# Optimization experiments

Measured on AMD Instinct MI355X. Metric: run time of the kernel, lower is better.

Reference implementation:

```python
import jax, jax.numpy as jnp
import numpy as np

NEG_SLOPE = 0.2


def gatv2(x, src, dst, eattr, Wl, bl, Wr, br, We, att, bias, concat):
    # GATv2Conv (PyG semantics): message j->i, softmax over incoming edges of target i.
    n = x.shape[0]
    H, C = att.shape
    xl = (x @ Wl + bl).reshape(n, H, C)   # source transform lin_l
    xr = (x @ Wr + br).reshape(n, H, C)   # target transform lin_r
    xe = (eattr @ We).reshape(-1, H, C)   # edge transform lin_edge (no bias)
    g = jax.nn.leaky_relu(xl[src] + xr[dst] + xe, NEG_SLOPE)  # [E,H,C]
    e = jnp.einsum('ehc,hc->eh', g, att)                      # [E,H]
    m = jax.ops.segment_max(e, dst, num_segments=n)
    a = jnp.exp(e - m[dst])
    s = jax.ops.segment_sum(a, dst, num_segments=n)
    alpha = a / (s[dst] + 1e-16)                              # [E,H]
    out = jax.ops.segment_sum(alpha[:, :, None] * xl[src], dst, num_segments=n)
    out = out.reshape(n, H * C) if concat else out.mean(axis=1)
    return out + bias, alpha


def add_self_loops(src, dst, eattr, n):
    # PyG default: add_self_loops=True, fill_value='mean' for edge_attr
    loop = jnp.arange(n, dtype=src.dtype)
    fill = jnp.broadcast_to(eattr.mean(axis=0, keepdims=True), (n, eattr.shape[1]))
    return (jnp.concatenate([src, loop]), jnp.concatenate([dst, loop]),
            jnp.concatenate([eattr, fill], axis=0))


def setup_inputs() -> dict:
    key = jax.random.key(0)
    ks = iter(jax.random.split(key, 64))
    B, N, D = 4, 2048, 256
    n = B * N
    E = 131072
    H, C1 = 4, 64  # conv1: heads=4, out=hidden//heads=64 (concat -> 256)
    C2 = 256       # conv2: heads=4, out=256, concat=False (mean)
    IN1 = 770

    def rn(shape, s=0.05):
        return jax.random.normal(next(ks), shape, dtype=jnp.float32) * s

    inp = {
        'h': rn((B, N, D), 1.0), 'c_temp': rn((B, N, D), 1.0),
        'c_stereo': rn((B, N, D), 1.0), 'e_proj': rn((B, N, 2), 1.0),
        'f_Lt': rn((B, N, D), 1.0),
        'edges': jax.random.randint(next(ks), (2, E), 0, n, dtype=jnp.int64),
        'edge_attr': rn((E, 1), 1.0),
        # conv1
        'Wl1': rn((IN1, H * C1)), 'bl1': jnp.zeros((H * C1,), jnp.float32),
        'Wr1': rn((IN1, H * C1)), 'br1': jnp.zeros((H * C1,), jnp.float32),
        'We1': rn((1, H * C1)), 'att1': rn((H, C1)),
        'bias1': jnp.zeros((H * C1,), jnp.float32),
        # conv2
        'Wl2': rn((D, H * C2)), 'bl2': jnp.zeros((H * C2,), jnp.float32),
        'Wr2': rn((D, H * C2)), 'br2': jnp.zeros((H * C2,), jnp.float32),
        'We2': rn((1, H * C2)), 'att2': rn((H, C2)),
        'bias2': jnp.zeros((C2,), jnp.float32),
        # GRUCell ([in, 3H] layout; gate order r,z,n as in torch)
        'Wih': rn((D, 3 * D)), 'bih': jnp.zeros((3 * D,), jnp.float32),
        'Whh': rn((D, 3 * D)), 'bhh': jnp.zeros((3 * D,), jnp.float32),
        # heads
        'rW1': rn((D, 256)), 'rb1': jnp.zeros((256,), jnp.float32),
        'rW2': rn((256, 2)), 'rb2': jnp.zeros((2,), jnp.float32),
        'wW1': rn((D, 256)), 'wb1': jnp.zeros((256,), jnp.float32),
        'wW2': rn((256, 2)), 'wb2': jnp.zeros((2,), jnp.float32),
        'pW1': rn((D, 128)), 'pb1': jnp.zeros((128,), jnp.float32),
        'pW2': rn((128, 1)), 'pb2': jnp.zeros((1,), jnp.float32),
        'dW1': rn((D, 128)), 'db1': jnp.zeros((128,), jnp.float32),
        'dW2': rn((128, 1)), 'db2': jnp.zeros((1,), jnp.float32),
    }
    return inp


def reference(h, c_temp, c_stereo, e_proj, f_Lt, edges, edge_attr,
              Wl1, bl1, Wr1, br1, We1, att1, bias1,
              Wl2, bl2, Wr2, br2, We2, att2, bias2,
              Wih, bih, Whh, bhh,
              rW1, rb1, rW2, rb2, wW1, wb1, wW2, wb2,
              pW1, pb1, pW2, pb2, dW1, db1, dW2, db2):
    B, N, D = f_Lt.shape
    n = B * N
    x = jnp.concatenate([c_temp, c_stereo, e_proj, f_Lt], axis=-1).reshape(n, -1)

    src, dst, ea = add_self_loops(edges[0], edges[1], edge_attr, n)
    x1, _ = gatv2(x, src, dst, ea, Wl1, bl1, Wr1, br1, We1, att1, bias1, concat=True)
    x1 = jax.nn.relu(x1)
    x2, alpha = gatv2(x1, src, dst, ea, Wl2, bl2, Wr2, br2, We2, att2, bias2, concat=False)

    # GRUCell
    hf = h.reshape(n, -1)
    gi = x2 @ Wih + bih
    gh = hf @ Whh + bhh
    ir, iz, inew = jnp.split(gi, 3, axis=-1)
    hr, hz, hnew = jnp.split(gh, 3, axis=-1)
    r_g = jax.nn.sigmoid(ir + hr)
    z_g = jax.nn.sigmoid(iz + hz)
    n_g = jnp.tanh(inew + r_g * hnew)
    h_new = ((1.0 - z_g) * n_g + z_g * hf).reshape(B, N, D)

    res = jax.nn.relu(h_new @ rW1 + rb1) @ rW2 + rb2
    w = jax.nn.sigmoid(jax.nn.relu(h_new @ wW1 + wb1) @ wW2 + wb2)
    a_p = jax.nn.softplus(jax.nn.relu(h_new @ pW1 + pb1) @ pW2 + pb2).mean(axis=1)
    a_d = jax.nn.softplus(jax.nn.relu(h_new @ dW1 + db1) @ dW2 + db2)
    return (h_new, res, w, a_p, a_d)
```

## Files before the change

### kernel.cpp

```cpp
#include <hip/hip_runtime.h>
#include <hip/hip_bf16.h>
#include <cstdint>
#include <cstddef>

#define N_NODES 8192
#define E_RAW   131072
#define E_TOT   (E_RAW + N_NODES)
#define HEADS   4

typedef __attribute__((ext_vector_type(8))) __bf16 bf16x8;
typedef __attribute__((ext_vector_type(4))) float f32x4;
typedef __attribute__((ext_vector_type(2))) float f32x2;

__device__ __forceinline__ void gload_lds16(const void* g, void* lds) {
  __builtin_amdgcn_global_load_lds(
      (const __attribute__((address_space(1))) unsigned int*)g,
      (__attribute__((address_space(3))) unsigned int*)lds, 16, 0, 0);
}

__device__ __forceinline__ float bfbits2f(unsigned short u) {
  return __uint_as_float((unsigned)u << 16);
}
__device__ __forceinline__ unsigned short f2bfbits(float f) {
  __hip_bfloat16 b = __float2bfloat16(f);
  return *(unsigned short*)&b;
}
__device__ __forceinline__ f32x2 unpk2(unsigned u) {
  return (f32x2){__uint_as_float(u << 16), __uint_as_float(u & 0xffff0000u)};
}
__device__ __forceinline__ unsigned char f32_to_fp8(float v) {
  int r = __builtin_amdgcn_cvt_pk_fp8_f32(v, v, 0, false);
  return (unsigned char)(r & 0xff);
}

__device__ __forceinline__ int eSrc(const int* __restrict__ src, int e) {
  return (e < E_RAW) ? src[e] : (e - E_RAW);
}
__device__ __forceinline__ int eDst(const int* __restrict__ dst, int e) {
  return (e < E_RAW) ? dst[e] : (e - E_RAW);
}


__global__ __launch_bounds__(256) void prep_kernel(
    const float* __restrict__ ct, const float* __restrict__ cs,
    const float* __restrict__ ep, const float* __restrict__ fl,
    const float* __restrict__ h, const float* __restrict__ ea,
    const float* bl1, const float* br1, const float* bl2, const float* br2,
    const float* rb1, const float* wb1, const float* pb1, const float* db1,
    __hip_bfloat16* __restrict__ x, __hip_bfloat16* __restrict__ Hb,
    float* __restrict__ MP, int* __restrict__ icnt_ipos,
    float* B1, float* B2, float* BH) {
  int blk = blockIdx.x;
  int tid = threadIdx.x;
  if (blk < 8192) {
    int i = blk;
    for (int j = tid; j < 832; j += 256) {
      float v;
      if (j < 256)      v = ct[(size_t)i * 256 + j];
      else if (j < 512) v = cs[(size_t)i * 256 + (j - 256)];
      else if (j < 514) v = ep[(size_t)i * 2 + (j - 512)];
      else if (j < 770) v = fl[(size_t)i * 256 + (j - 514)];
      else              v = 0.f;
      x[(size_t)i * 832 + j] = __float2bfloat16(v);
    }
  } else if (blk < 9216) {
    size_t base = ((size_t)(blk - 8192) * 256 + tid) * 8;
    float4 a = *(const float4*)(h + base);
    float4 b = *(const float4*)(h + base + 4);
    unsigned short o[8];
    o[0]=f2bfbits(a.x); o[1]=f2bfbits(a.y); o[2]=f2bfbits(a.z); o[3]=f2bfbits(a.w);
    o[4]=f2bfbits(b.x); o[5]=f2bfbits(b.y); o[6]=f2bfbits(b.z); o[7]=f2bfbits(b.w);
    *(uint4*)((unsigned short*)Hb + base) = *(uint4*)o;
  } else if (blk < 9472) {
    __shared__ float sm[256];
    int bb = blk - 9216;
    float acc = 0.f;
    for (int i = bb * 256 + tid; i < E_RAW; i += 256 * 256) acc += ea[i];
    sm[tid] = acc; __syncthreads();
    for (int s = 128; s; s >>= 1) { if (tid < s) sm[tid] += sm[tid + s]; __syncthreads(); }
    if (tid == 0) MP[bb] = sm[0];
  } else if (blk < 9536) {
    int i = (blk - 9472) * 256 + tid;
    if (i < 2 * N_NODES) icnt_ipos[i] = 0;
  } else {
    int i = (blk - 9536) * 256 + tid;
    if (i < 512) B1[i] = (i < 256) ? bl1[i] : br1[i - 256];
    else if (i < 2560) { int k = i - 512; B2[k] = (k < 1024) ? bl2[k] : br2[k - 1024]; }
    else if (i < 3328) {
      int k = i - 2560;
      BH[k] = (k < 256) ? rb1[k] : (k < 512) ? wb1[k - 256] : (k < 640) ? pb1[k - 512] : db1[k - 640];
    }
  }
}


__global__ void csr_count(const int* __restrict__ dst, int* __restrict__ cnt) {
  int e = blockIdx.x * blockDim.x + threadIdx.x;
  if (e < E_TOT) atomicAdd(&cnt[eDst(dst, e)], 1);
}

__global__ __launch_bounds__(1024) void csr_scan(const int* __restrict__ cnt,
                                                 int* __restrict__ off,
                                                 float* __restrict__ MP) {
  __shared__ int part[1024];
  __shared__ float sm[256];
  int t = threadIdx.x;
  if (t < 256) sm[t] = MP[t];
  __syncthreads();
  for (int s = 128; s; s >>= 1) { if (t < s) sm[t] += sm[t + s]; __syncthreads(); }
  if (t == 0) MP[256] = sm[0] * (1.f / (float)E_RAW);
  int base = t * 8;
  int loc[8];
  int s = 0;
#pragma unroll
  for (int i = 0; i < 8; ++i) { loc[i] = s; s += cnt[base + i]; }
  part[t] = s; __syncthreads();
  for (int d = 1; d < 1024; d <<= 1) {
    int v = (t >= d) ? part[t - d] : 0;
    __syncthreads();
    part[t] += v;
    __syncthreads();
  }
  int pre = (t == 0) ? 0 : part[t - 1];
#pragma unroll
  for (int i = 0; i < 8; ++i) off[base + i] = pre + loc[i];
  if (t == 1023) off[8192] = part[1023];
}

__global__ void csr_fill(const int* __restrict__ src, const int* __restrict__ dst,
                         const float* __restrict__ ea, const float* __restrict__ eamean,
                         const int* __restrict__ off, int* __restrict__ pos,
                         int* __restrict__ srcn, float* __restrict__ eav) {
  int e = blockIdx.x * blockDim.x + threadIdx.x;
  if (e >= E_TOT) return;
  int d = eDst(dst, e);
  int p = off[d] + atomicAdd(&pos[d], 1);
  srcn[p] = eSrc(src, e);
  eav[p] = (e < E_RAW) ? ea[e] : eamean[0];
}


__global__ __launch_bounds__(256) void wt_all(
    const float* w0, const float* w1, const float* w2, const float* w3,
    const float* w4, const float* w5, const float* w6, const float* w7,
    const float* w8, const float* w9,
    __hip_bfloat16* WT1, __hip_bfloat16* WT2, __hip_bfloat16* WTih,
    __hip_bfloat16* WThh, __hip_bfloat16* WTh) {
  const int cum[10] = {208, 416, 672, 928, 1120, 1312, 1376, 1440, 1472, 1504};
  const int Kt[10]  = {770, 770, 256, 256, 256, 256, 256, 256, 256, 256};
  const int Nt[10]  = {256, 256, 1024, 1024, 768, 768, 256, 256, 128, 128};
  const int KPt[10] = {832, 832, 256, 256, 256, 256, 256, 256, 256, 256};
  const int n0t[10] = {0, 256, 0, 1024, 0, 0, 0, 256, 512, 640};
  int job = 0;
  while (blockIdx.x >= (unsigned)cum[job]) ++job;
  int lb = blockIdx.x - (job ? cum[job - 1] : 0);
  int K = Kt[job], N = Nt[job], KP = KPt[job], n0 = n0t[job];
  int tilesX = KP >> 5;
  int k0 = (lb % tilesX) * 32, nb = (lb / tilesX) * 32;
  const float* W;
  switch (job) {
    case 0: W = w0; break; case 1: W = w1; break; case 2: W = w2; break;
    case 3: W = w3; break; case 4: W = w4; break; case 5: W = w5; break;
    case 6: W = w6; break; case 7: W = w7; break; case 8: W = w8; break;
    default: W = w9; break;
  }
  __hip_bfloat16* WT = (job < 2) ? WT1 : (job < 4) ? WT2 : (job == 4) ? WTih
                       : (job == 5) ? WThh : WTh;
  __shared__ float sm[32][33];
  int tx = threadIdx.x & 31, ty = threadIdx.x >> 5;
  for (int yy = ty; yy < 32; yy += 8) {
    int k = k0 + yy, n = nb + tx;
    sm[yy][tx] = (k < K && n < N) ? W[(size_t)k * N + n] : 0.f;
  }
  __syncthreads();
  for (int yy = ty; yy < 32; yy += 8) {
    int n = nb + yy, k = k0 + tx;
    if (n < N) WT[(size_t)(n0 + n) * KP + k] = __float2bfloat16(sm[tx][yy]);
  }
}


template <int OUT>
__global__ __launch_bounds__(512) void mfma_gemm(
    const __hip_bfloat16* __restrict__ A, const __hip_bfloat16* __restrict__ BT,
    const float* __restrict__ bias, void* __restrict__ Cout, int KP, int N,
    const __hip_bfloat16* A2, const __hip_bfloat16* BT2,
    const float* bias2, void* C2, unsigned char* __restrict__ Cfp8) {
  if (blockIdx.z == 1) { A = A2; BT = BT2; bias = bias2; Cout = C2; }
  __shared__ uint4 AsBuf[1024];
  __shared__ uint4 BsBuf[1024];
  char* Asc = (char*)AsBuf;
  char* Bsc = (char*)BsBuf;
  int tid = threadIdx.x;
  int lane = tid & 63;
  int wid = tid >> 6;
  int wr = wid >> 1;
  int wc = wid & 1;
  int bm = blockIdx.y * 128;
  int bn = blockIdx.x * 128;
  f32x4 acc[2][4];
#pragma unroll
  for (int i = 0; i < 2; ++i)
#pragma unroll
    for (int j = 0; j < 4; ++j) acc[i][j] = (f32x4){0.f, 0.f, 0.f, 0.f};

  int nK = KP >> 6;
  for (int kt = 0; kt < nK; ++kt) {
    int k0 = kt * 64;
#pragma unroll
    for (int i = 0; i < 2; ++i) {
      int p = i * 512 + tid;
      int row = p >> 3, cc = p & 7;
      int sc = cc ^ (row & 7);
      gload_lds16(A + (size_t)(bm + row) * KP + k0 + sc * 8, Asc + p * 16);
      gload_lds16(BT + (size_t)(bn + row) * KP + k0 + sc * 8, Bsc + p * 16);
    }
    __syncthreads();
#pragma unroll
    for (int s = 0; s < 2; ++s) {
      bf16x8 af[2], bfr[4];
#pragma unroll
      for (int f = 0; f < 2; ++f) {
        int r = wr * 32 + f * 16 + (lane & 15);
        int ch = (s * 4 + (lane >> 4)) ^ (r & 7);
        af[f] = *(const bf16x8*)(Asc + r * 128 + ch * 16);
      }
#pragma unroll
      for (int f = 0; f < 4; ++f) {
        int n = wc * 64 + f * 16 + (lane & 15);
        int cb = (s * 4 + (lane >> 4)) ^ (n & 7);
        bfr[f] = *(const bf16x8*)(Bsc + n * 128 + cb * 16);
      }
#pragma unroll
      for (int fm = 0; fm < 2; ++fm)
#pragma unroll
        for (int fn = 0; fn < 4; ++fn)
          acc[fm][fn] = __builtin_amdgcn_mfma_f32_16x16x32_bf16(af[fm], bfr[fn], acc[fm][fn], 0, 0, 0);
    }
    __syncthreads();
  }
  int rbase = bm + wr * 32 + (lane >> 4) * 4;
  int cbase = bn + wc * 64 + (lane & 15);
#pragma unroll
  for (int fm = 0; fm < 2; ++fm)
#pragma unroll
    for (int fn = 0; fn < 4; ++fn) {
      int col = cbase + fn * 16;
      float bv = bias[col];
#pragma unroll
      for (int j = 0; j < 4; ++j) {
        int row = rbase + fm * 16 + j;
        float v = acc[fm][fn][j] + bv;
        if (OUT == 2 || OUT == 3) v = fmaxf(v, 0.f);
        if (OUT == 0 || OUT == 3 || OUT == 4)
          ((__hip_bfloat16*)Cout)[(size_t)row * N + col] = __float2bfloat16(v);
        else
          ((float*)Cout)[(size_t)row * N + col] = v;
        if (OUT == 4 && col < 1024)
          Cfp8[(size_t)row * 1024 + col] = f32_to_fp8(v);
      }
    }
}


__global__ __launch_bounds__(256) void gat_fused1(
    const __hip_bfloat16* __restrict__ XLR,
    const int* __restrict__ off, const int* __restrict__ srcn,
    const float* __restrict__ eav, const float* __restrict__ We,
    const float* __restrict__ att, const float* __restrict__ bias,
    __hip_bfloat16* __restrict__ X1) {
  int d = (blockIdx.x * 256 + threadIdx.x) >> 6;
  int lane = threadIdx.x & 63;
  int q = lane & 15;
  int j0 = (lane >> 4) * 64 + q * 4;
  const unsigned short* X = (const unsigned short*)XLR;
  uint2 xv = *(const uint2*)(X + (size_t)d * 512 + 256 + j0);
  f32x2 xr[2] = {unpk2(xv.x), unpk2(xv.y)};
  f32x2 we[2] = {*(const f32x2*)(We + j0), *(const f32x2*)(We + j0 + 2)};
  f32x2 at[2] = {*(const f32x2*)(att + j0), *(const f32x2*)(att + j0 + 2)};
  int b = off[d], e1 = off[d + 1], pe = e1 - 1;
  int sB = srcn[b]; float eaA = eav[b];
  uint2 vA = *(const uint2*)(X + (size_t)sB * 512 + j0);
  int p1 = min(b + 1, pe); sB = srcn[p1]; float eaB = eav[p1];
  float m = -INFINITY, ss = 0.f;
  f32x2 a[2] = {(f32x2){0.f, 0.f}, (f32x2){0.f, 0.f}};
  for (int p = b; p < e1; ++p) {
    uint2 vu = vA; float ea = eaA; eaA = eaB;
    vA = *(const uint2*)(X + (size_t)sB * 512 + j0);
    int p2 = min(p + 2, pe); sB = srcn[p2]; eaB = eav[p2];
    f32x2 v[2] = {unpk2(vu.x), unpk2(vu.y)};
    f32x2 ea2 = (f32x2){ea, ea};
    f32x2 t2 = (f32x2){0.f, 0.f};
#pragma unroll
    for (int i = 0; i < 2; ++i) {
      f32x2 gg = (v[i] + xr[i]) + ea2 * we[i];
      f32x2 lr = __builtin_elementwise_max(gg, 0.2f * gg);
      t2 = t2 + lr * at[i];
    }
    float t = t2.x + t2.y;
    t += __shfl_xor(t, 8, 64); t += __shfl_xor(t, 4, 64);
    t += __shfl_xor(t, 2, 64); t += __shfl_xor(t, 1, 64);
    if (__all(t <= m)) {
      float wp = __expf(t - m);
      ss += wp;
      f32x2 wp2 = (f32x2){wp, wp};
#pragma unroll
      for (int i = 0; i < 2; ++i) a[i] = a[i] + wp2 * v[i];
    } else {
      float mn = fmaxf(m, t);
      float scl = __expf(m - mn);
      float wp = __expf(t - mn);
      ss = fmaf(ss, scl, wp);
      f32x2 wp2 = (f32x2){wp, wp}, s2 = (f32x2){scl, scl};
#pragma unroll
      for (int i = 0; i < 2; ++i) a[i] = a[i] * s2 + wp2 * v[i];
      m = mn;
    }
  }
  float inv = 1.f / (ss + 1e-16f);
  unsigned short o[4];
  o[0] = f2bfbits(fmaxf(fmaf(a[0].x, inv, bias[j0]), 0.f));
  o[1] = f2bfbits(fmaxf(fmaf(a[0].y, inv, bias[j0 + 1]), 0.f));
  o[2] = f2bfbits(fmaxf(fmaf(a[1].x, inv, bias[j0 + 2]), 0.f));
  o[3] = f2bfbits(fmaxf(fmaf(a[1].y, inv, bias[j0 + 3]), 0.f));
  *(uint2*)((unsigned short*)X1 + (size_t)d * 256 + j0) = *(uint2*)o;
}


__global__ __launch_bounds__(256) void gat_fused2(
    const unsigned char* __restrict__ XL8,
    const __hip_bfloat16* __restrict__ XLR,
    const int* __restrict__ off, const int* __restrict__ srcn,
    const float* __restrict__ eav, const float* __restrict__ We,
    const float* __restrict__ att, const float* __restrict__ bias,
    __hip_bfloat16* __restrict__ X2) {
  int d = (blockIdx.x * 256 + threadIdx.x) >> 6;
  int lane = threadIdx.x & 63;
  int g = lane >> 4, q = lane & 15;
  int j0 = g * 256 + q * 16;
  const unsigned short* X = (const unsigned short*)XLR;
  f32x2 xr[8], we[8], at[8], a[8];
  {
    const uint4* xp = (const uint4*)(X + (size_t)d * 2048 + 1024 + j0);
    uint4 r0 = xp[0], r1 = xp[1];
    xr[0] = unpk2(r0.x); xr[1] = unpk2(r0.y); xr[2] = unpk2(r0.z); xr[3] = unpk2(r0.w);
    xr[4] = unpk2(r1.x); xr[5] = unpk2(r1.y); xr[6] = unpk2(r1.z); xr[7] = unpk2(r1.w);
#pragma unroll
    for (int i = 0; i < 8; ++i) {
      we[i] = *(const f32x2*)(We + j0 + 2 * i);
      at[i] = *(const f32x2*)(att + j0 + 2 * i);
      a[i] = (f32x2){0.f, 0.f};
    }
  }
  int b = off[d], e1 = off[d + 1], pe = e1 - 1;
  int sB = srcn[b]; float eaA = eav[b];
  uint4 rA = *(const uint4*)(XL8 + (size_t)sB * 1024 + j0);
  int p1 = min(b + 1, pe); sB = srcn[p1]; float eaB = eav[p1];
  float m = -INFINITY, ss = 0.f;
  for (int p = b; p < e1; ++p) {
    uint4 cc = rA; float ea = eaA; eaA = eaB;
    rA = *(const uint4*)(XL8 + (size_t)sB * 1024 + j0);
    int p2 = min(p + 2, pe); sB = srcn[p2]; eaB = eav[p2];
    f32x2 v[8];
    v[0] = (f32x2){__builtin_amdgcn_cvt_f32_fp8(cc.x, 0), __builtin_amdgcn_cvt_f32_fp8(cc.x, 1)};
    v[1] = (f32x2){__builtin_amdgcn_cvt_f32_fp8(cc.x, 2), __builtin_amdgcn_cvt_f32_fp8(cc.x, 3)};
    v[2] = (f32x2){__builtin_amdgcn_cvt_f32_fp8(cc.y, 0), __builtin_amdgcn_cvt_f32_fp8(cc.y, 1)};
    v[3] = (f32x2){__builtin_amdgcn_cvt_f32_fp8(cc.y, 2), __builtin_amdgcn_cvt_f32_fp8(cc.y, 3)};
    v[4] = (f32x2){__builtin_amdgcn_cvt_f32_fp8(cc.z, 0), __builtin_amdgcn_cvt_f32_fp8(cc.z, 1)};
    v[5] = (f32x2){__builtin_amdgcn_cvt_f32_fp8(cc.z, 2), __builtin_amdgcn_cvt_f32_fp8(cc.z, 3)};
    v[6] = (f32x2){__builtin_amdgcn_cvt_f32_fp8(cc.w, 0), __builtin_amdgcn_cvt_f32_fp8(cc.w, 1)};
    v[7] = (f32x2){__builtin_amdgcn_cvt_f32_fp8(cc.w, 2), __builtin_amdgcn_cvt_f32_fp8(cc.w, 3)};
    f32x2 ea2 = (f32x2){ea, ea};
    f32x2 t2 = (f32x2){0.f, 0.f};
#pragma unroll
    for (int i = 0; i < 8; ++i) {
      f32x2 gg = (v[i] + xr[i]) + ea2 * we[i];
      f32x2 lr = __builtin_elementwise_max(gg, 0.2f * gg);
      t2 = t2 + lr * at[i];
    }
    float t = t2.x + t2.y;
    t += __shfl_xor(t, 8, 64); t += __shfl_xor(t, 4, 64);
    t += __shfl_xor(t, 2, 64); t += __shfl_xor(t, 1, 64);
    if (__all(t <= m)) {
      float wp = __expf(t - m);
      ss += wp;
      f32x2 wp2 = (f32x2){wp, wp};
#pragma unroll
      for (int i = 0; i < 8; ++i) a[i] = a[i] + wp2 * v[i];
    } else {
      float mn = fmaxf(m, t);
      float scl = __expf(m - mn);
      float wp = __expf(t - mn);
      ss = fmaf(ss, scl, wp);
      f32x2 wp2 = (f32x2){wp, wp}, s2 = (f32x2){scl, scl};
#pragma unroll
      for (int i = 0; i < 8; ++i) a[i] = a[i] * s2 + wp2 * v[i];
      m = mn;
    }
  }
  float inv = 1.f / (ss + 1e-16f);
  f32x2 inv2 = (f32x2){inv, inv};
#pragma unroll
  for (int i = 0; i < 8; ++i) {
    f32x2 r2 = a[i] * inv2;
    r2.x += __shfl_xor(r2.x, 16, 64);
    r2.x += __shfl_xor(r2.x, 32, 64);
    r2.y += __shfl_xor(r2.y, 16, 64);
    r2.y += __shfl_xor(r2.y, 32, 64);
    a[i] = r2;
  }
  if (g == 0) {
    unsigned short o[16];
#pragma unroll
    for (int i = 0; i < 8; ++i) {
      o[2 * i]     = f2bfbits(fmaf(0.25f, a[i].x, bias[q * 16 + 2 * i]));
      o[2 * i + 1] = f2bfbits(fmaf(0.25f, a[i].y, bias[q * 16 + 2 * i + 1]));
    }
    uint4* op = (uint4*)((unsigned short*)X2 + (size_t)d * 256 + q * 16);
    op[0] = ((uint4*)o)[0];
    op[1] = ((uint4*)o)[1];
  }
}


__global__ void gru_kernel(const __hip_bfloat16* __restrict__ gi,
                           const __hip_bfloat16* __restrict__ gh,
                           const float* __restrict__ hf, float* __restrict__ hn,
                           __hip_bfloat16* __restrict__ hnb) {
  int i = blockIdx.x;
  int c = threadIdx.x;
  size_t b = (size_t)i * 768;
  const unsigned short* giu = (const unsigned short*)gi;
  const unsigned short* ghu = (const unsigned short*)gh;
  float ir = bfbits2f(giu[b + c]), iz = bfbits2f(giu[b + 256 + c]), in_ = bfbits2f(giu[b + 512 + c]);
  float hr = bfbits2f(ghu[b + c]), hz = bfbits2f(ghu[b + 256 + c]), hn_ = bfbits2f(ghu[b + 512 + c]);
  float r = 1.f / (1.f + __expf(-(ir + hr)));
  float z = 1.f / (1.f + __expf(-(iz + hz)));
  float ng = tanhf(in_ + r * hn_);
  float h0 = hf[(size_t)i * 256 + c];
  float v = (1.f - z) * ng + z * h0;
  hn[(size_t)i * 256 + c] = v;
  hnb[(size_t)i * 256 + c] = __float2bfloat16(v);
}


__global__ __launch_bounds__(256) void heads_final(
    const __hip_bfloat16* __restrict__ Tb,
    const float* __restrict__ rW2, const float* __restrict__ rb2,
    const float* __restrict__ wW2, const float* __restrict__ wb2,
    const float* __restrict__ pW2, const float* __restrict__ pb2,
    const float* __restrict__ dW2, const float* __restrict__ db2,
    float* __restrict__ o_res, float* __restrict__ o_w,
    float* __restrict__ AP, float* __restrict__ o_ad) {
  int node = (blockIdx.x * 256 + threadIdx.x) >> 6;
  int lane = threadIdx.x & 63;
  const unsigned short* t = (const unsigned short*)Tb + (size_t)node * 768;
  ushort4 tr = *(const ushort4*)(t + lane * 4);
  ushort4 tw = *(const ushort4*)(t + 256 + lane * 4);
  float trf[4] = {bfbits2f(tr.x), bfbits2f(tr.y), bfbits2f(tr.z), bfbits2f(tr.w)};
  float twf[4] = {bfbits2f(tw.x), bfbits2f(tw.y), bfbits2f(tw.z), bfbits2f(tw.w)};
  float tpf[4] = {0.f, 0.f, 0.f, 0.f}, tdf[4] = {0.f, 0.f, 0.f, 0.f};
  if (lane < 32) {
    ushort4 tp = *(const ushort4*)(t + 512 + lane * 4);
    ushort4 td = *(const ushort4*)(t + 640 + lane * 4);
    tpf[0] = bfbits2f(tp.x); tpf[1] = bfbits2f(tp.y); tpf[2] = bfbits2f(tp.z); tpf[3] = bfbits2f(tp.w);
    tdf[0] = bfbits2f(td.x); tdf[1] = bfbits2f(td.y); tdf[2] = bfbits2f(td.z); tdf[3] = bfbits2f(td.w);
  }
  float r0 = 0.f, r1 = 0.f, w0 = 0.f, w1 = 0.f, pp = 0.f, dd = 0.f;
#pragma unroll
  for (int i = 0; i < 4; ++i) {
    int k = lane * 4 + i;
    r0 = fmaf(trf[i], rW2[k * 2], r0);
    r1 = fmaf(trf[i], rW2[k * 2 + 1], r1);
    w0 = fmaf(twf[i], wW2[k * 2], w0);
    w1 = fmaf(twf[i], wW2[k * 2 + 1], w1);
  }
  if (lane < 32) {
#pragma unroll
    for (int i = 0; i < 4; ++i) {
      int k = lane * 4 + i;
      pp = fmaf(tpf[i], pW2[k], pp);
      dd = fmaf(tdf[i], dW2[k], dd);
    }
  }
#pragma unroll
  for (int o = 32; o; o >>= 1) {
    r0 += __shfl_xor(r0, o, 64); r1 += __shfl_xor(r1, o, 64);
    w0 += __shfl_xor(w0, o, 64); w1 += __shfl_xor(w1, o, 64);
    pp += __shfl_xor(pp, o, 64); dd += __shfl_xor(dd, o, 64);
  }
  if (lane == 0) {
    o_res[(size_t)node * 2]     = r0 + rb2[0];
    o_res[(size_t)node * 2 + 1] = r1 + rb2[1];
    float sw0 = w0 + wb2[0], sw1 = w1 + wb2[1];
    o_w[(size_t)node * 2]     = 1.f / (1.f + __expf(-sw0));
    o_w[(size_t)node * 2 + 1] = 1.f / (1.f + __expf(-sw1));
    float vp = pp + pb2[0];
    AP[node] = fmaxf(vp, 0.f) + log1pf(__expf(-fabsf(vp)));
    float vd = dd + db2[0];
    o_ad[node] = fmaxf(vd, 0.f) + log1pf(__expf(-fabsf(vd)));
  }
}

__global__ void ap_reduce(const float* __restrict__ ap, float* __restrict__ out) {
  __shared__ float sm[256];
  int b = blockIdx.x, tid = threadIdx.x;
  float acc = 0.f;
  for (int i = tid; i < 2048; i += 256) acc += ap[b * 2048 + i];
  sm[tid] = acc; __syncthreads();
  for (int s = 128; s; s >>= 1) { if (tid < s) sm[tid] += sm[tid + s]; __syncthreads(); }
  if (tid == 0) out[b] = sm[0] * (1.f / 2048.f);
}


extern "C" void kernel_launch(void* const* d_in, const int* in_sizes, int n_in,
                              void* d_out, int out_size, void* d_ws, size_t ws_size,
                              hipStream_t stream) {
  const float* h        = (const float*)d_in[0];
  const float* c_temp   = (const float*)d_in[1];
  const float* c_stereo = (const float*)d_in[2];
  const float* e_proj   = (const float*)d_in[3];
  const float* f_Lt     = (const float*)d_in[4];
  const int*   edges    = (const int*)d_in[5];
  const float* eattr    = (const float*)d_in[6];
  const float* Wl1 = (const float*)d_in[7];  const float* bl1 = (const float*)d_in[8];
  const float* Wr1 = (const float*)d_in[9];  const float* br1 = (const float*)d_in[10];
  const float* We1 = (const float*)d_in[11]; const float* att1 = (const float*)d_in[12];
  const float* bias1 = (const float*)d_in[13];
  const float* Wl2 = (const float*)d_in[14]; const float* bl2 = (const float*)d_in[15];
  const float* Wr2 = (const float*)d_in[16]; const float* br2 = (const float*)d_in[17];
  const float* We2 = (const float*)d_in[18]; const float* att2 = (const float*)d_in[19];
  const float* bias2 = (const float*)d_in[20];
  const float* Wih = (const float*)d_in[21]; const float* bih = (const float*)d_in[22];
  const float* Whh = (const float*)d_in[23]; const float* bhh = (const float*)d_in[24];
  const float* rW1 = (const float*)d_in[25]; const float* rb1 = (const float*)d_in[26];
  const float* rW2 = (const float*)d_in[27]; const float* rb2 = (const float*)d_in[28];
  const float* wW1 = (const float*)d_in[29]; const float* wb1 = (const float*)d_in[30];
  const float* wW2 = (const float*)d_in[31]; const float* wb2 = (const float*)d_in[32];
  const float* pW1 = (const float*)d_in[33]; const float* pb1 = (const float*)d_in[34];
  const float* pW2 = (const float*)d_in[35]; const float* pb2 = (const float*)d_in[36];
  const float* dW1 = (const float*)d_in[37]; const float* db1 = (const float*)d_in[38];
  const float* dW2 = (const float*)d_in[39]; const float* db2 = (const float*)d_in[40];

  const int* src = edges;
  const int* dst = edges + E_RAW;

  float* base = (float*)d_ws;
  size_t cur = 0;
  auto alloc = [&](size_t n) { float* p = base + cur; cur += (n + 63) & ~(size_t)63; return p; };

  float* BIG0 = alloc(8388608);
  float* BIG1 = alloc(6291456);
  float* XLR1f = alloc(2097152);
  float* XL8f = alloc(2097152);
  float* X1f  = alloc(1048576);
  float* X2f  = alloc(1048576);
  float* Hbf  = alloc(1048576);
  float* HNbf = alloc(1048576);
  float* WT1f = alloc(212992);
  float* WT2f = alloc(262144);
  float* WTihf = alloc(98304);
  float* WThhf = alloc(98304);
  float* WThf  = alloc(98304);
  float* B1 = alloc(512);
  float* B2 = alloc(2048);
  float* BH = alloc(768);
  float* EAV = alloc(E_TOT);
  float* AP  = alloc(N_NODES);
  float* MP  = alloc(320);
  int* ICNT = (int*)alloc(2 * N_NODES);
  int* IOFF = (int*)alloc(N_NODES + 64);
  int* ISRC = (int*)alloc(E_TOT);
  if (ws_size < cur * 4) return;
  int* IPOS = ICNT + N_NODES;

  __hip_bfloat16* x_bf = (__hip_bfloat16*)BIG1;
  __hip_bfloat16* XLR1 = (__hip_bfloat16*)XLR1f;
  __hip_bfloat16* XLR2 = (__hip_bfloat16*)BIG0;
  unsigned char* XL8 = (unsigned char*)XL8f;
  __hip_bfloat16* X1b = (__hip_bfloat16*)X1f;
  __hip_bfloat16* X2b = (__hip_bfloat16*)X2f;
  __hip_bfloat16* Hb  = (__hip_bfloat16*)Hbf;
  __hip_bfloat16* HNb = (__hip_bfloat16*)HNbf;
  __hip_bfloat16* WT1 = (__hip_bfloat16*)WT1f;
  __hip_bfloat16* WT2 = (__hip_bfloat16*)WT2f;
  __hip_bfloat16* WTih = (__hip_bfloat16*)WTihf;
  __hip_bfloat16* WThh = (__hip_bfloat16*)WThhf;
  __hip_bfloat16* WTh  = (__hip_bfloat16*)WThf;
  __hip_bfloat16* gi = (__hip_bfloat16*)BIG0;
  __hip_bfloat16* gh = (__hip_bfloat16*)BIG1;
  __hip_bfloat16* Tb = (__hip_bfloat16*)BIG0;

  float* o_hnew = (float*)d_out;
  float* o_res  = o_hnew + (size_t)N_NODES * 256;
  float* o_w    = o_res + (size_t)N_NODES * 2;
  float* o_ap   = o_w + (size_t)N_NODES * 2;
  float* o_ad   = o_ap + 4;

  prep_kernel<<<9549, 256, 0, stream>>>(c_temp, c_stereo, e_proj, f_Lt, h, eattr,
                                        bl1, br1, bl2, br2, rb1, wb1, pb1, db1,
                                        x_bf, Hb, MP, ICNT, B1, B2, BH);
  csr_count<<<(E_TOT + 255) / 256, 256, 0, stream>>>(dst, ICNT);
  csr_scan<<<1, 1024, 0, stream>>>(ICNT, IOFF, MP);
  csr_fill<<<(E_TOT + 255) / 256, 256, 0, stream>>>(src, dst, eattr, MP + 256,
                                                    IOFF, IPOS, ISRC, EAV);
  wt_all<<<1504, 256, 0, stream>>>(Wl1, Wr1, Wl2, Wr2, Wih, Whh, rW1, wW1, pW1, dW1,
                                   WT1, WT2, WTih, WThh, WTh);

  mfma_gemm<0><<<dim3(4, 64, 1), 512, 0, stream>>>(x_bf, WT1, B1, XLR1, 832, 512,
                                                   nullptr, nullptr, nullptr, nullptr, nullptr);
  gat_fused1<<<N_NODES / 4, 256, 0, stream>>>(XLR1, IOFF, ISRC, EAV, We1, att1, bias1, X1b);

  mfma_gemm<4><<<dim3(16, 64, 1), 512, 0, stream>>>(X1b, WT2, B2, XLR2, 256, 2048,
                                                    nullptr, nullptr, nullptr, nullptr, XL8);
  gat_fused2<<<N_NODES / 4, 256, 0, stream>>>(XL8, XLR2, IOFF, ISRC, EAV, We2, att2, bias2, X2b);

  mfma_gemm<0><<<dim3(6, 64, 2), 512, 0, stream>>>(X2b, WTih, bih, gi, 256, 768,
                                                   Hb, WThh, bhh, gh, nullptr);
  gru_kernel<<<N_NODES, 256, 0, stream>>>(gi, gh, h, o_hnew, HNb);

  mfma_gemm<3><<<dim3(6, 64, 1), 512, 0, stream>>>(HNb, WTh, BH, Tb, 256, 768,
                                                   nullptr, nullptr, nullptr, nullptr, nullptr);
  heads_final<<<N_NODES / 4, 256, 0, stream>>>(Tb, rW2, rb2, wW2, wb2, pW2, pb2, dW2, db2,
                                               o_res, o_w, AP, o_ad);
  ap_reduce<<<4, 256, 0, stream>>>(AP, o_ap);
}
```

Measured before the change: 207.1 us.

## Gather fp8 source features in first GAT layer and unroll edge loops by two

New measurement: 208.4 us. No clear change (+0.6%).

```diff
diff --git a/kernel.cpp b/kernel.cpp
--- a/kernel.cpp
+++ b/kernel.cpp
@@ -251,19 +251,19 @@
       for (int j = 0; j < 4; ++j) {
         int row = rbase + fm * 16 + j;
         float v = acc[fm][fn][j] + bv;
-        if (OUT == 2 || OUT == 3) v = fmaxf(v, 0.f);
-        if (OUT == 0 || OUT == 3 || OUT == 4)
-          ((__hip_bfloat16*)Cout)[(size_t)row * N + col] = __float2bfloat16(v);
-        else
-          ((float*)Cout)[(size_t)row * N + col] = v;
+        if (OUT == 3) v = fmaxf(v, 0.f);
+        ((__hip_bfloat16*)Cout)[(size_t)row * N + col] = __float2bfloat16(v);
         if (OUT == 4 && col < 1024)
           Cfp8[(size_t)row * 1024 + col] = f32_to_fp8(v);
+        if (OUT == 5 && col < 256)
+          Cfp8[(size_t)row * 256 + col] = f32_to_fp8(v);
       }
     }
 }
 
 
 __global__ __launch_bounds__(256) void gat_fused1(
+    const unsigned char* __restrict__ XL8,
     const __hip_bfloat16* __restrict__ XLR,
     const int* __restrict__ off, const int* __restrict__ srcn,
     const float* __restrict__ eav, const float* __restrict__ We,
@@ -279,16 +279,13 @@
   f32x2 we[2] = {*(const f32x2*)(We + j0), *(const f32x2*)(We + j0 + 2)};
   f32x2 at[2] = {*(const f32x2*)(att + j0), *(const f32x2*)(att + j0 + 2)};
   int b = off[d], e1 = off[d + 1], pe = e1 - 1;
-  int sB = srcn[b]; float eaA = eav[b];
-  uint2 vA = *(const uint2*)(X + (size_t)sB * 512 + j0);
-  int p1 = min(b + 1, pe); sB = srcn[p1]; float eaB = eav[p1];
   float m = -INFINITY, ss = 0.f;
   f32x2 a[2] = {(f32x2){0.f, 0.f}, (f32x2){0.f, 0.f}};
-  for (int p = b; p < e1; ++p) {
-    uint2 vu = vA; float ea = eaA; eaA = eaB;
-    vA = *(const uint2*)(X + (size_t)sB * 512 + j0);
-    int p2 = min(p + 2, pe); sB = srcn[p2]; eaB = eav[p2];
-    f32x2 v[2] = {unpk2(vu.x), unpk2(vu.y)};
+
+  auto proc = [&](unsigned cc, float ea, bool valid) {
+    f32x2 v[2];
+    v[0] = (f32x2){__builtin_amdgcn_cvt_f32_fp8(cc, 0), __builtin_amdgcn_cvt_f32_fp8(cc, 1)};
+    v[1] = (f32x2){__builtin_amdgcn_cvt_f32_fp8(cc, 2), __builtin_amdgcn_cvt_f32_fp8(cc, 3)};
     f32x2 ea2 = (f32x2){ea, ea};
     f32x2 t2 = (f32x2){0.f, 0.f};
 #pragma unroll
@@ -300,6 +297,7 @@
     float t = t2.x + t2.y;
     t += __shfl_xor(t, 8, 64); t += __shfl_xor(t, 4, 64);
     t += __shfl_xor(t, 2, 64); t += __shfl_xor(t, 1, 64);
+    if (!valid) t = -1e30f;
     if (__all(t <= m)) {
       float wp = __expf(t - m);
       ss += wp;
@@ -316,6 +314,27 @@
       for (int i = 0; i < 2; ++i) a[i] = a[i] * s2 + wp2 * v[i];
       m = mn;
     }
+  };
+
+  int i1 = min(b + 1, pe);
+  int s0 = srcn[b], s1 = srcn[i1];
+  float ea0 = eav[b], ea1 = eav[i1];
+  unsigned r0 = *(const unsigned*)(XL8 + (size_t)s0 * 256 + j0);
+  unsigned r1 = *(const unsigned*)(XL8 + (size_t)s1 * 256 + j0);
+  int i2 = min(b + 2, pe), i3 = min(b + 3, pe);
+  int s2i = srcn[i2], s3i = srcn[i3];
+  float ea2 = eav[i2], ea3 = eav[i3];
+  for (int p = b; p < e1; p += 2) {
+    unsigned c0 = r0, c1 = r1;
+    float ce0 = ea0, ce1 = ea1;
+    r0 = *(const unsigned*)(XL8 + (size_t)s2i * 256 + j0);
+    r1 = *(const unsigned*)(XL8 + (size_t)s3i * 256 + j0);
+    ea0 = ea2; ea1 = ea3;
+    int i4 = min(p + 4, pe), i5 = min(p + 5, pe);
+    s2i = srcn[i4]; s3i = srcn[i5];
+    ea2 = eav[i4]; ea3 = eav[i5];
+    proc(c0, ce0, true);
+    proc(c1, ce1, p + 1 < e1);
   }
   float inv = 1.f / (ss + 1e-16f);
   unsigned short o[4];
@@ -353,14 +372,9 @@
     }
   }
   int b = off[d], e1 = off[d + 1], pe = e1 - 1;
-  int sB = srcn[b]; float eaA = eav[b];
-  uint4 rA = *(const uint4*)(XL8 + (size_t)sB * 1024 + j0);
-  int p1 = min(b + 1, pe); sB = srcn[p1]; float eaB = eav[p1];
   float m = -INFINITY, ss = 0.f;
-  for (int p = b; p < e1; ++p) {
-    uint4 cc = rA; float ea = eaA; eaA = eaB;
-    rA = *(const uint4*)(XL8 + (size_t)sB * 1024 + j0);
-    int p2 = min(p + 2, pe); sB = srcn[p2]; eaB = eav[p2];
+
+  auto proc = [&](uint4 cc, float ea, bool valid) {
     f32x2 v[8];
     v[0] = (f32x2){__builtin_amdgcn_cvt_f32_fp8(cc.x, 0), __builtin_amdgcn_cvt_f32_fp8(cc.x, 1)};
     v[1] = (f32x2){__builtin_amdgcn_cvt_f32_fp8(cc.x, 2), __builtin_amdgcn_cvt_f32_fp8(cc.x, 3)};
@@ -381,6 +395,7 @@
     float t = t2.x + t2.y;
     t += __shfl_xor(t, 8, 64); t += __shfl_xor(t, 4, 64);
     t += __shfl_xor(t, 2, 64); t += __shfl_xor(t, 1, 64);
+    if (!valid) t = -1e30f;
     if (__all(t <= m)) {
       float wp = __expf(t - m);
       ss += wp;
@@ -397,6 +412,27 @@
       for (int i = 0; i < 8; ++i) a[i] = a[i] * s2 + wp2 * v[i];
       m = mn;
     }
+  };
+
+  int i1 = min(b + 1, pe);
+  int s0 = srcn[b], s1 = srcn[i1];
+  float ea0 = eav[b], ea1 = eav[i1];
+  uint4 r0 = *(const uint4*)(XL8 + (size_t)s0 * 1024 + j0);
+  uint4 r1 = *(const uint4*)(XL8 + (size_t)s1 * 1024 + j0);
+  int i2 = min(b + 2, pe), i3 = min(b + 3, pe);
+  int s2i = srcn[i2], s3i = srcn[i3];
+  float ea2 = eav[i2], ea3 = eav[i3];
+  for (int p = b; p < e1; p += 2) {
+    uint4 c0 = r0, c1 = r1;
+    float ce0 = ea0, ce1 = ea1;
+    r0 = *(const uint4*)(XL8 + (size_t)s2i * 1024 + j0);
+    r1 = *(const uint4*)(XL8 + (size_t)s3i * 1024 + j0);
+    ea0 = ea2; ea1 = ea3;
+    int i4 = min(p + 4, pe), i5 = min(p + 5, pe);
+    s2i = srcn[i4]; s3i = srcn[i5];
+    ea2 = eav[i4]; ea3 = eav[i5];
+    proc(c0, ce0, true);
+    proc(c1, ce1, p + 1 < e1);
   }
   float inv = 1.f / (ss + 1e-16f);
   f32x2 inv2 = (f32x2){inv, inv};
@@ -553,6 +589,7 @@
   float* BIG1 = alloc(6291456);
   float* XLR1f = alloc(2097152);
   float* XL8f = alloc(2097152);
+  float* XL81f = alloc(524288);
   float* X1f  = alloc(1048576);
   float* X2f  = alloc(1048576);
   float* Hbf  = alloc(1048576);
@@ -578,6 +615,7 @@
   __hip_bfloat16* XLR1 = (__hip_bfloat16*)XLR1f;
   __hip_bfloat16* XLR2 = (__hip_bfloat16*)BIG0;
   unsigned char* XL8 = (unsigned char*)XL8f;
+  unsigned char* XL81 = (unsigned char*)XL81f;
   __hip_bfloat16* X1b = (__hip_bfloat16*)X1f;
   __hip_bfloat16* X2b = (__hip_bfloat16*)X2f;
   __hip_bfloat16* Hb  = (__hip_bfloat16*)Hbf;
@@ -607,9 +645,9 @@
   wt_all<<<1504, 256, 0, stream>>>(Wl1, Wr1, Wl2, Wr2, Wih, Whh, rW1, wW1, pW1, dW1,
                                    WT1, WT2, WTih, WThh, WTh);
 
-  mfma_gemm<0><<<dim3(4, 64, 1), 512, 0, stream>>>(x_bf, WT1, B1, XLR1, 832, 512,
-                                                   nullptr, nullptr, nullptr, nullptr, nullptr);
-  gat_fused1<<<N_NODES / 4, 256, 0, stream>>>(XLR1, IOFF, ISRC, EAV, We1, att1, bias1, X1b);
+  mfma_gemm<5><<<dim3(4, 64, 1), 512, 0, stream>>>(x_bf, WT1, B1, XLR1, 832, 512,
+                                                   nullptr, nullptr, nullptr, nullptr, XL81);
+  gat_fused1<<<N_NODES / 4, 256, 0, stream>>>(XL81, XLR1, IOFF, ISRC, EAV, We1, att1, bias1, X1b);
 
   mfma_gemm<4><<<dim3(16, 64, 1), 512, 0, stream>>>(X1b, WT2, B2, XLR2, 256, 2048,
                                                     nullptr, nullptr, nullptr, nullptr, XL8);
```

## Fuse GRU gate GEMMs with cell update and gather FP8 source features in GAT1

Applied to the files above, without the earlier changes.

New measurement: 201.7 us, median of 2. -2.6%, faster.

```diff
diff --git a/kernel.cpp b/kernel.cpp
--- a/kernel.cpp
+++ b/kernel.cpp
@@ -184,9 +184,7 @@
 __global__ __launch_bounds__(512) void mfma_gemm(
     const __hip_bfloat16* __restrict__ A, const __hip_bfloat16* __restrict__ BT,
     const float* __restrict__ bias, void* __restrict__ Cout, int KP, int N,
-    const __hip_bfloat16* A2, const __hip_bfloat16* BT2,
-    const float* bias2, void* C2, unsigned char* __restrict__ Cfp8) {
-  if (blockIdx.z == 1) { A = A2; BT = BT2; bias = bias2; Cout = C2; }
+    unsigned char* __restrict__ Cfp8) {
   __shared__ uint4 AsBuf[1024];
   __shared__ uint4 BsBuf[1024];
   char* Asc = (char*)AsBuf;
@@ -251,19 +249,24 @@
       for (int j = 0; j < 4; ++j) {
         int row = rbase + fm * 16 + j;
         float v = acc[fm][fn][j] + bv;
-        if (OUT == 2 || OUT == 3) v = fmaxf(v, 0.f);
-        if (OUT == 0 || OUT == 3 || OUT == 4)
+        if (OUT == 3) v = fmaxf(v, 0.f);
+        if (OUT == 0 || OUT == 3)
           ((__hip_bfloat16*)Cout)[(size_t)row * N + col] = __float2bfloat16(v);
-        else
-          ((float*)Cout)[(size_t)row * N + col] = v;
-        if (OUT == 4 && col < 1024)
-          Cfp8[(size_t)row * 1024 + col] = f32_to_fp8(v);
+        if (OUT == 6) {
+          if (col < 256) Cfp8[(size_t)row * 256 + col] = f32_to_fp8(v);
+          else ((__hip_bfloat16*)Cout)[(size_t)row * N + col] = __float2bfloat16(v);
+        }
+        if (OUT == 7) {
+          if (col < 1024) Cfp8[(size_t)row * 1024 + col] = f32_to_fp8(v);
+          else ((__hip_bfloat16*)Cout)[(size_t)row * N + col] = __float2bfloat16(v);
+        }
       }
     }
 }
 
 
 __global__ __launch_bounds__(256) void gat_fused1(
+    const unsigned char* __restrict__ XL8,
     const __hip_bfloat16* __restrict__ XLR,
     const int* __restrict__ off, const int* __restrict__ srcn,
     const float* __restrict__ eav, const float* __restrict__ We,
@@ -280,15 +283,17 @@
   f32x2 at[2] = {*(const f32x2*)(att + j0), *(const f32x2*)(att + j0 + 2)};
   int b = off[d], e1 = off[d + 1], pe = e1 - 1;
   int sB = srcn[b]; float eaA = eav[b];
-  uint2 vA = *(const uint2*)(X + (size_t)sB * 512 + j0);
+  unsigned rA = *(const unsigned*)(XL8 + (size_t)sB * 256 + j0);
   int p1 = min(b + 1, pe); sB = srcn[p1]; float eaB = eav[p1];
   float m = -INFINITY, ss = 0.f;
   f32x2 a[2] = {(f32x2){0.f, 0.f}, (f32x2){0.f, 0.f}};
   for (int p = b; p < e1; ++p) {
-    uint2 vu = vA; float ea = eaA; eaA = eaB;
-    vA = *(const uint2*)(X + (size_t)sB * 512 + j0);
+    unsigned cc = rA; float ea = eaA; eaA = eaB;
+    rA = *(const unsigned*)(XL8 + (size_t)sB * 256 + j0);
     int p2 = min(p + 2, pe); sB = srcn[p2]; eaB = eav[p2];
-    f32x2 v[2] = {unpk2(vu.x), unpk2(vu.y)};
+    f32x2 v[2];
+    v[0] = (f32x2){__builtin_amdgcn_cvt_f32_fp8(cc, 0), __builtin_amdgcn_cvt_f32_fp8(cc, 1)};
+    v[1] = (f32x2){__builtin_amdgcn_cvt_f32_fp8(cc, 2), __builtin_amdgcn_cvt_f32_fp8(cc, 3)};
     f32x2 ea2 = (f32x2){ea, ea};
     f32x2 t2 = (f32x2){0.f, 0.f};
 #pragma unroll
@@ -423,24 +428,104 @@
 }
 
 
-__global__ void gru_kernel(const __hip_bfloat16* __restrict__ gi,
-                           const __hip_bfloat16* __restrict__ gh,
-                           const float* __restrict__ hf, float* __restrict__ hn,
-                           __hip_bfloat16* __restrict__ hnb) {
-  int i = blockIdx.x;
-  int c = threadIdx.x;
-  size_t b = (size_t)i * 768;
-  const unsigned short* giu = (const unsigned short*)gi;
-  const unsigned short* ghu = (const unsigned short*)gh;
-  float ir = bfbits2f(giu[b + c]), iz = bfbits2f(giu[b + 256 + c]), in_ = bfbits2f(giu[b + 512 + c]);
-  float hr = bfbits2f(ghu[b + c]), hz = bfbits2f(ghu[b + 256 + c]), hn_ = bfbits2f(ghu[b + 512 + c]);
-  float r = 1.f / (1.f + __expf(-(ir + hr)));
-  float z = 1.f / (1.f + __expf(-(iz + hz)));
-  float ng = tanhf(in_ + r * hn_);
-  float h0 = hf[(size_t)i * 256 + c];
-  float v = (1.f - z) * ng + z * h0;
-  hn[(size_t)i * 256 + c] = v;
-  hnb[(size_t)i * 256 + c] = __float2bfloat16(v);
+__global__ __launch_bounds__(512) void gru_gemm(
+    const __hip_bfloat16* __restrict__ X2b,
+    const __hip_bfloat16* __restrict__ Hb,
+    const __hip_bfloat16* __restrict__ WTih,
+    const __hip_bfloat16* __restrict__ WThh,
+    const float* __restrict__ bih, const float* __restrict__ bhh,
+    const float* __restrict__ hf,
+    float* __restrict__ hn, __hip_bfloat16* __restrict__ hnb) {
+  __shared__ uint4 AxB[512];
+  __shared__ uint4 AhB[512];
+  __shared__ uint4 BiB[1024];
+  __shared__ uint4 BhB[1024];
+  char* Ax = (char*)AxB;
+  char* Ah = (char*)AhB;
+  char* Bi = (char*)BiB;
+  char* Bh = (char*)BhB;
+  int tid = threadIdx.x;
+  int lane = tid & 63, wid = tid >> 6;
+  int wr = wid >> 1, wc = wid & 1;
+  int bm = blockIdx.y * 64;
+  int c0 = blockIdx.x * 128;
+  float rv[16], zv[16];
+  float outv[16];
+  for (int gate = 0; gate < 3; ++gate) {
+    f32x4 ai[4], ah[4];
+#pragma unroll
+    for (int j = 0; j < 4; ++j) { ai[j] = (f32x4){0.f,0.f,0.f,0.f}; ah[j] = (f32x4){0.f,0.f,0.f,0.f}; }
+    for (int kt = 0; kt < 4; ++kt) {
+      int k0 = kt * 64;
+      {
+        int p = tid;
+        int row = p >> 3, cc = p & 7;
+        int sc = cc ^ (row & 7);
+        gload_lds16(X2b + (size_t)(bm + row) * 256 + k0 + sc * 8, Ax + p * 16);
+        gload_lds16(Hb + (size_t)(bm + row) * 256 + k0 + sc * 8, Ah + p * 16);
+      }
+#pragma unroll
+      for (int i = 0; i < 2; ++i) {
+        int p = i * 512 + tid;
+        int row = p >> 3, cc = p & 7;
+        int sc = cc ^ (row & 7);
+        int n = gate * 256 + c0 + row;
+        gload_lds16(WTih + (size_t)n * 256 + k0 + sc * 8, Bi + p * 16);
+        gload_lds16(WThh + (size_t)n * 256 + k0 + sc * 8, Bh + p * 16);
+      }
+      __syncthreads();
+#pragma unroll
+      for (int s = 0; s < 2; ++s) {
+        int rl = wr * 16 + (lane & 15);
+        int ch = (s * 4 + (lane >> 4)) ^ (rl & 7);
+        bf16x8 axf = *(const bf16x8*)(Ax + rl * 128 + ch * 16);
+        bf16x8 ahf = *(const bf16x8*)(Ah + rl * 128 + ch * 16);
+        bf16x8 bif[4], bhf[4];
+#pragma unroll
+        for (int f = 0; f < 4; ++f) {
+          int nl = wc * 64 + f * 16 + (lane & 15);
+          int cb = (s * 4 + (lane >> 4)) ^ (nl & 7);
+          bif[f] = *(const bf16x8*)(Bi + nl * 128 + cb * 16);
+          bhf[f] = *(const bf16x8*)(Bh + nl * 128 + cb * 16);
+        }
+#pragma unroll
+        for (int fn = 0; fn < 4; ++fn) {
+          ai[fn] = __builtin_amdgcn_mfma_f32_16x16x32_bf16(axf, bif[fn], ai[fn], 0, 0, 0);
+          ah[fn] = __builtin_amdgcn_mfma_f32_16x16x32_bf16(ahf, bhf[fn], ah[fn], 0, 0, 0);
+        }
+      }
+      __syncthreads();
+    }
+#pragma unroll
+    for (int fn = 0; fn < 4; ++fn) {
+      int colL = wc * 64 + fn * 16 + (lane & 15);
+      int ng = gate * 256 + c0 + colL;
+      float bi_v = bih[ng], bh_v = bhh[ng];
+#pragma unroll
+      for (int j = 0; j < 4; ++j) {
+        int k = fn * 4 + j;
+        float vi = ai[fn][j] + bi_v;
+        float vh = ah[fn][j] + bh_v;
+        if (gate == 0) rv[k] = 1.f / (1.f + __expf(-(vi + vh)));
+        else if (gate == 1) zv[k] = 1.f / (1.f + __expf(-(vi + vh)));
+        else outv[k] = tanhf(vi + rv[k] * vh);
+      }
+    }
+  }
+#pragma unroll
+  for (int fn = 0; fn < 4; ++fn) {
+    int colL = wc * 64 + fn * 16 + (lane & 15);
+    int chn = c0 + colL;
+#pragma unroll
+    for (int j = 0; j < 4; ++j) {
+      int k = fn * 4 + j;
+      int row = bm + wr * 16 + (lane >> 4) * 4 + j;
+      float h0 = hf[(size_t)row * 256 + chn];
+      float v = (1.f - zv[k]) * outv[k] + zv[k] * h0;
+      hn[(size_t)row * 256 + chn] = v;
+      hnb[(size_t)row * 256 + chn] = __float2bfloat16(v);
+    }
+  }
 }
 
 
@@ -553,6 +638,7 @@
   float* BIG1 = alloc(6291456);
   float* XLR1f = alloc(2097152);
   float* XL8f = alloc(2097152);
+  float* XL81f = alloc(524288);
   float* X1f  = alloc(1048576);
   float* X2f  = alloc(1048576);
   float* Hbf  = alloc(1048576);
@@ -578,6 +664,7 @@
   __hip_bfloat16* XLR1 = (__hip_bfloat16*)XLR1f;
   __hip_bfloat16* XLR2 = (__hip_bfloat16*)BIG0;
   unsigned char* XL8 = (unsigned char*)XL8f;
+  unsigned char* XL81 = (unsigned char*)XL81f;
   __hip_bfloat16* X1b = (__hip_bfloat16*)X1f;
   __hip_bfloat16* X2b = (__hip_bfloat16*)X2f;
   __hip_bfloat16* Hb  = (__hip_bfloat16*)Hbf;
@@ -587,8 +674,6 @@
   __hip_bfloat16* WTih = (__hip_bfloat16*)WTihf;
   __hip_bfloat16* WThh = (__hip_bfloat16*)WThhf;
   __hip_bfloat16* WTh  = (__hip_bfloat16*)WThf;
-  __hip_bfloat16* gi = (__hip_bfloat16*)BIG0;
-  __hip_bfloat16* gh = (__hip_bfloat16*)BIG1;
   __hip_bfloat16* Tb = (__hip_bfloat16*)BIG0;
 
   float* o_hnew = (float*)d_out;
@@ -607,20 +692,15 @@
   wt_all<<<1504, 256, 0, stream>>>(Wl1, Wr1, Wl2, Wr2, Wih, Whh, rW1, wW1, pW1, dW1,
                                    WT1, WT2, WTih, WThh, WTh);
 
-  mfma_gemm<0><<<dim3(4, 64, 1), 512, 0, stream>>>(x_bf, WT1, B1, XLR1, 832, 512,
-                                                   nullptr, nullptr, nullptr, nullptr, nullptr);
-  gat_fused1<<<N_NODES / 4, 256, 0, stream>>>(XLR1, IOFF, ISRC, EAV, We1, att1, bias1, X1b);
-
-  mfma_gemm<4><<<dim3(16, 64, 1), 512, 0, stream>>>(X1b, WT2, B2, XLR2, 256, 2048,
-                                                    nullptr, nullptr, nullptr, nullptr, XL8);
+  mfma_gemm<6><<<dim3(4, 64), 512, 0, stream>>>(x_bf, WT1, B1, XLR1, 832, 512, XL81);
+  gat_fused1<<<N_NODES / 4, 256, 0, stream>>>(XL81, XLR1, IOFF, ISRC, EAV, We1, att1, bias1, X1b);
+
+  mfma_gemm<7><<<dim3(16, 64), 512, 0, stream>>>(X1b, WT2, B2, XLR2, 256, 2048, XL8);
   gat_fused2<<<N_NODES / 4, 256, 0, stream>>>(XL8, XLR2, IOFF, ISRC, EAV, We2, att2, bias2, X2b);
 
-  mfma_gemm<0><<<dim3(6, 64, 2), 512, 0, stream>>>(X2b, WTih, bih, gi, 256, 768,
-                                                   Hb, WThh, bhh, gh, nullptr);
-  gru_kernel<<<N_NODES, 256, 0, stream>>>(gi, gh, h, o_hnew, HNb);
-
-  mfma_gemm<3><<<dim3(6, 64, 1), 512, 0, stream>>>(HNb, WTh, BH, Tb, 256, 768,
-                                                   nullptr, nullptr, nullptr, nullptr, nullptr);
+  gru_gemm<<<dim3(2, 128), 512, 0, stream>>>(X2b, Hb, WTih, WThh, bih, bhh, h, o_hnew, HNb);
+
+  mfma_gemm<3><<<dim3(6, 64), 512, 0, stream>>>(HNb, WTh, BH, Tb, 256, 768, nullptr);
   heads_final<<<N_NODES / 4, 256, 0, stream>>>(Tb, rW2, rb2, wW2, wb2, pW2, pb2, dW2, db2,
                                                o_res, o_w, AP, o_ad);
   ap_reduce<<<4, 256, 0, stream>>>(AP, o_ap);
```
